# Kernel tuning notes

Measured on AMD Instinct MI355X. Metric: run time of the kernel, lower is better.

## Reference

```python
import jax, jax.numpy as jnp
import numpy as np

LN2 = float(np.log(2.0))

def ssp(x):
    # ShiftedSoftplus: softplus(x) - log(2)
    return jax.nn.softplus(x) - LN2

N_NODES = 40000
N_EDGES = 640000
HIDDEN = 128
N_FILTERS = 128
N_GAUSS = 50
CUTOFF = 10.0

def setup_inputs() -> dict:
    key = jax.random.key(0)
    ks = jax.random.split(key, 12)
    s = 0.05
    x = jax.random.normal(ks[0], (N_NODES, HIDDEN), dtype=jnp.float32)
    edge_index = jax.random.randint(ks[1], (2, N_EDGES), 0, N_NODES)
    edge_weight = jax.random.uniform(ks[2], (N_EDGES,), dtype=jnp.float32) * CUTOFF
    edge_attr = jax.random.normal(ks[3], (N_EDGES, N_GAUSS), dtype=jnp.float32)
    # filter MLP params (Linear(num_gaussians,num_filters), ssp, Linear(num_filters,num_filters))
    mlp_w1 = jax.random.normal(ks[4], (N_FILTERS, N_GAUSS), dtype=jnp.float32) * s
    mlp_b1 = jnp.zeros((N_FILTERS,), dtype=jnp.float32)
    mlp_w2 = jax.random.normal(ks[5], (N_FILTERS, N_FILTERS), dtype=jnp.float32) * s
    mlp_b2 = jnp.zeros((N_FILTERS,), dtype=jnp.float32)
    # CFConv linears: lin1 (no bias), lin2 (bias)
    lin1_w = jax.random.normal(ks[6], (N_FILTERS, HIDDEN), dtype=jnp.float32) * s
    lin2_w = jax.random.normal(ks[7], (HIDDEN, N_FILTERS), dtype=jnp.float32) * s
    lin2_b = jnp.zeros((HIDDEN,), dtype=jnp.float32)
    # output linear
    lin_w = jax.random.normal(ks[8], (HIDDEN, HIDDEN), dtype=jnp.float32) * s
    lin_b = jnp.zeros((HIDDEN,), dtype=jnp.float32)
    return {
        "x": x, "edge_index": edge_index, "edge_weight": edge_weight, "edge_attr": edge_attr,
        "mlp_w1": mlp_w1, "mlp_b1": mlp_b1, "mlp_w2": mlp_w2, "mlp_b2": mlp_b2,
        "lin1_w": lin1_w, "lin2_w": lin2_w, "lin2_b": lin2_b,
        "lin_w": lin_w, "lin_b": lin_b,
    }

def reference(x, edge_index, edge_weight, edge_attr,
              mlp_w1, mlp_b1, mlp_w2, mlp_b2,
              lin1_w, lin2_w, lin2_b, lin_w, lin_b):
    src, dst = edge_index[0], edge_index[1]
    # cosine envelope
    C = 0.5 * (jnp.cos(edge_weight * jnp.pi / CUTOFF) + 1.0)  # (E,)
    # filter MLP on Gaussian-smeared distances
    W = ssp(edge_attr @ mlp_w1.T + mlp_b1) @ mlp_w2.T + mlp_b2  # (E, F)
    W = W * C[:, None]
    # CFConv: lin1 -> gather x_j -> multiply -> scatter-add -> lin2
    h = x @ lin1_w.T                                            # (N, F)
    msg = h[src] * W                                            # (E, F)
    agg = jax.ops.segment_sum(msg, dst, num_segments=x.shape[0])  # (N, F)
    h2 = agg @ lin2_w.T + lin2_b                                # (N, H)
    # activation + output projection
    out = ssp(h2) @ lin_w.T + lin_b                             # (N, H)
    return out
```

## Files before the change

### kernel.cpp

```cpp
#include <hip/hip_runtime.h>
#include <math.h>

#define LN2F 0.69314718055994531f

typedef _Float16 v8hf __attribute__((ext_vector_type(8)));
typedef _Float16 v2hf __attribute__((ext_vector_type(2)));
typedef float    v4f  __attribute__((ext_vector_type(4)));

__device__ __forceinline__ float ssp_fast(float x) {
    float e = __expf(-fabsf(x));
    return fmaxf(x, 0.f) + __logf(1.f + e) - LN2F;
}

__global__ __launch_bounds__(256)
void prep_kernel(const float* __restrict__ w1, const float* __restrict__ w2,
                 const float* __restrict__ l1w, const float* __restrict__ l2w,
                 const float* __restrict__ lw,
                 _Float16* __restrict__ w1f, _Float16* __restrict__ w2f,
                 _Float16* __restrict__ l1f, _Float16* __restrict__ l2f,
                 _Float16* __restrict__ lwf)
{
    int idx = blockIdx.x * 256 + threadIdx.x;
    if (idx < 8192) {
        int i = idx & 7, lane = (idx >> 3) & 63, ks = (idx >> 9) & 1, nt = idx >> 10;
        int r = nt * 16 + (lane & 15);
        int k = ks * 32 + (lane >> 4) * 8 + i;
        w1f[idx] = (k < 50) ? (_Float16)w1[r * 50 + k] : (_Float16)0.f;
        return;
    }
    int o = idx - 8192;
    if (o >= 4 * 16384) return;
    int which = o >> 14;
    int p = o & 16383;
    int i = p & 7, lane = (p >> 3) & 63, ks = (p >> 9) & 3, nt = p >> 11;
    int r = nt * 16 + (lane & 15);
    int k = ks * 32 + (lane >> 4) * 8 + i;
    const float* src = (which == 0) ? w2 : (which == 1) ? l1w : (which == 2) ? l2w : lw;
    _Float16* dst   = (which == 0) ? w2f : (which == 1) ? l1f : (which == 2) ? l2f : lwf;
    dst[p] = (_Float16)src[r * 128 + k];
}

__global__ __launch_bounds__(256)
void h_gemm_kernel(const float* __restrict__ X, const _Float16* __restrict__ Wf,
                   float* __restrict__ Y, int M)
{
    const int tid = threadIdx.x, lane = tid & 63, wv = tid >> 6;
    const int l15 = lane & 15, quad = lane >> 4;
    const int mb = blockIdx.x * 64 + wv * 16;

    const int mA = (mb + l15 < M) ? (mb + l15) : (M - 1);
    v8hf a[4];
    #pragma unroll
    for (int ks = 0; ks < 4; ++ks) {
        const float4* xp = (const float4*)&X[(size_t)mA * 128 + ks * 32 + quad * 8];
        float4 x0 = xp[0], x1 = xp[1];
        v8hf t = {(_Float16)x0.x, (_Float16)x0.y, (_Float16)x0.z, (_Float16)x0.w,
                  (_Float16)x1.x, (_Float16)x1.y, (_Float16)x1.z, (_Float16)x1.w};
        a[ks] = t;
    }
    #pragma unroll
    for (int nt = 0; nt < 8; ++nt) {
        v4f acc = {0.f, 0.f, 0.f, 0.f};
        #pragma unroll
        for (int ks = 0; ks < 4; ++ks) {
            const v8hf b = *(const v8hf*)&Wf[((nt * 4 + ks) * 64 + lane) * 8];
            acc = __builtin_amdgcn_mfma_f32_16x16x32_f16(a[ks], b, acc, 0, 0, 0);
        }
        const int col = nt * 16 + l15;
        #pragma unroll
        for (int r = 0; r < 4; ++r) {
            int row = mb + quad * 4 + r;
            if (row < M) Y[(size_t)row * 128 + col] = acc[r];
        }
    }
}

__global__ __launch_bounds__(256)
void fused_out_kernel(const float* __restrict__ agg, const _Float16* __restrict__ l2f,
                      const float* __restrict__ l2b, const _Float16* __restrict__ lwf,
                      const float* __restrict__ lb, float* __restrict__ out, int M)
{
    __shared__ __align__(16) _Float16 Sh[64 * 138];
    const int tid = threadIdx.x, lane = tid & 63, wv = tid >> 6;
    const int l15 = lane & 15, quad = lane >> 4;
    const int m0 = wv * 16;
    const int gbase = blockIdx.x * 64;

    const int mA = (gbase + m0 + l15 < M) ? (gbase + m0 + l15) : (M - 1);
    v8hf a[4];
    #pragma unroll
    for (int ks = 0; ks < 4; ++ks) {
        const float4* xp = (const float4*)&agg[(size_t)mA * 128 + ks * 32 + quad * 8];
        float4 x0 = xp[0], x1 = xp[1];
        v8hf t = {(_Float16)x0.x, (_Float16)x0.y, (_Float16)x0.z, (_Float16)x0.w,
                  (_Float16)x1.x, (_Float16)x1.y, (_Float16)x1.z, (_Float16)x1.w};
        a[ks] = t;
    }
    #pragma unroll
    for (int nt = 0; nt < 8; ++nt) {
        v4f acc = {0.f, 0.f, 0.f, 0.f};
        #pragma unroll
        for (int ks = 0; ks < 4; ++ks) {
            const v8hf b = *(const v8hf*)&l2f[((nt * 4 + ks) * 64 + lane) * 8];
            acc = __builtin_amdgcn_mfma_f32_16x16x32_f16(a[ks], b, acc, 0, 0, 0);
        }
        const float bj = l2b[nt * 16 + l15];
        #pragma unroll
        for (int r = 0; r < 4; ++r)
            Sh[(m0 + quad * 4 + r) * 138 + nt * 16 + l15] =
                (_Float16)ssp_fast(acc[r] + bj);
    }
    v8hf ua[4];
    #pragma unroll
    for (int ks = 0; ks < 4; ++ks)
        ua[ks] = *(const v8hf*)&Sh[(m0 + l15) * 138 + ks * 32 + quad * 8];

    #pragma unroll
    for (int nt = 0; nt < 8; ++nt) {
        v4f acc = {0.f, 0.f, 0.f, 0.f};
        #pragma unroll
        for (int ks = 0; ks < 4; ++ks) {
            const v8hf b = *(const v8hf*)&lwf[((nt * 4 + ks) * 64 + lane) * 8];
            acc = __builtin_amdgcn_mfma_f32_16x16x32_f16(ua[ks], b, acc, 0, 0, 0);
        }
        const int col = nt * 16 + l15;
        const float bj = lb[col];
        #pragma unroll
        for (int r = 0; r < 4; ++r) {
            int row = gbase + m0 + quad * 4 + r;
            if (row < M) out[(size_t)row * 128 + col] = acc[r] + bj;
        }
    }
}

template<int MODE>
__global__ __launch_bounds__(256, 5)
void edge_kernel(const float* __restrict__ attr,
                 const float* __restrict__ ew,
                 const int* __restrict__ srcI,
                 const int* __restrict__ dstI,
                 const _Float16* __restrict__ w1f,
                 const _Float16* __restrict__ w2f,
                 const float* __restrict__ b1,
                 const float* __restrict__ b2,
                 const float* __restrict__ h,
                 float* __restrict__ agg,
                 float* __restrict__ msg32,
                 _Float16* __restrict__ msg16,
                 int E)
{
    __shared__ __align__(16) _Float16 Af[64 * 64];
    __shared__ __align__(16) _Float16 Uh[64 * 138];

    const int tid = threadIdx.x;
    const int e_base = blockIdx.x * 64;
    const int lane = tid & 63, wv = tid >> 6;
    const int m0 = wv * 16, l15 = lane & 15, quad = lane >> 4;

    float cC[4]; const float* hrow[4]; float* arow[4]; bool val[4]; int eidx[4];
    #pragma unroll
    for (int r = 0; r < 4; ++r) {
        int eg = e_base + m0 + quad * 4 + r;
        val[r] = eg < E;
        eidx[r] = eg;
        int e = val[r] ? eg : (E - 1);
        cC[r] = 0.5f * (__cosf(ew[e] * 0.31415926535897932f) + 1.f);
        hrow[r] = h + (size_t)srcI[e] * 128;
        if constexpr (MODE == 0) arow[r] = agg + (size_t)dstI[e] * 128;
    }

    for (int idx = tid; idx < 4096; idx += 256) {
        int r = idx >> 6, g = idx & 63;
        int e = e_base + r;
        float v = (g < 50 && e < E) ? attr[(size_t)e * 50 + g] : 0.f;
        Af[((((r >> 4) * 2 + (g >> 5)) * 64) + (((g & 31) >> 3) * 16) + (r & 15)) * 8
           + (g & 7)] = (_Float16)v;
    }
    __syncthreads();

    float hv[8][4];
    #pragma unroll
    for (int nt = 0; nt < 8; ++nt)
        #pragma unroll
        for (int r = 0; r < 4; ++r)
            hv[nt][r] = hrow[r][nt * 16 + l15];

    const v8hf a0 = *(const v8hf*)&Af[((wv * 2 + 0) * 64 + lane) * 8];
    const v8hf a1 = *(const v8hf*)&Af[((wv * 2 + 1) * 64 + lane) * 8];
    #pragma unroll
    for (int nt = 0; nt < 8; ++nt) {
        v4f acc = {0.f, 0.f, 0.f, 0.f};
        const v8hf bA = *(const v8hf*)&w1f[((nt * 2 + 0) * 64 + lane) * 8];
        const v8hf bB = *(const v8hf*)&w1f[((nt * 2 + 1) * 64 + lane) * 8];
        acc = __builtin_amdgcn_mfma_f32_16x16x32_f16(a0, bA, acc, 0, 0, 0);
        acc = __builtin_amdgcn_mfma_f32_16x16x32_f16(a1, bB, acc, 0, 0, 0);
        const float bj = b1[nt * 16 + l15];
        #pragma unroll
        for (int r = 0; r < 4; ++r)
            Uh[(m0 + quad * 4 + r) * 138 + nt * 16 + l15] =
                (_Float16)ssp_fast(acc[r] + bj);
    }

    v8hf ua[4];
    #pragma unroll
    for (int ks = 0; ks < 4; ++ks)
        ua[ks] = *(const v8hf*)&Uh[(m0 + l15) * 138 + ks * 32 + quad * 8];

    #pragma unroll
    for (int nt = 0; nt < 8; ++nt) {
        v4f acc = {0.f, 0.f, 0.f, 0.f};
        #pragma unroll
        for (int ks = 0; ks < 4; ++ks) {
            const v8hf b = *(const v8hf*)&w2f[((nt * 4 + ks) * 64 + lane) * 8];
            acc = __builtin_amdgcn_mfma_f32_16x16x32_f16(ua[ks], b, acc, 0, 0, 0);
        }
        const int col = nt * 16 + l15;
        const float bj = b2[col];
        #pragma unroll
        for (int r = 0; r < 4; ++r) {
            if (val[r]) {
                float m = (acc[r] + bj) * cC[r] * hv[nt][r];
                if constexpr (MODE == 0)
                    atomicAdd(&arow[r][col], m);
                else if constexpr (MODE == 1)
                    msg32[(size_t)eidx[r] * 128 + col] = m;
                else
                    msg16[(size_t)eidx[r] * 128 + col] = (_Float16)m;
            }
        }
    }
}

__global__ __launch_bounds__(256)
void hist_kernel(const int* __restrict__ dst, int* __restrict__ counts, int E)
{
    int i = blockIdx.x * 256 + threadIdx.x;
    const int stride = gridDim.x * 256;
    for (; i < E; i += stride) atomicAdd(&counts[dst[i]], 1);
}

__global__ __launch_bounds__(256)
void scan1_kernel(int* __restrict__ data, int* __restrict__ bsum, int N)
{
    __shared__ int wsum[4];
    const int t = threadIdx.x, lane = t & 63, wv = t >> 6;
    const int base = blockIdx.x * 1024 + t * 4;
    int v0 = 0, v1 = 0, v2 = 0, v3 = 0;
    if (base + 0 < N) v0 = data[base + 0];
    if (base + 1 < N) v1 = data[base + 1];
    if (base + 2 < N) v2 = data[base + 2];
    if (base + 3 < N) v3 = data[base + 3];
    const int s = v0 + v1 + v2 + v3;
    int sc = s;
    #pragma unroll
    for (int d = 1; d < 64; d <<= 1) {
        int o = __shfl_up(sc, d);
        if (lane >= d) sc += o;
    }
    if (lane == 63) wsum[wv] = sc;
    __syncthreads();
    int wo = 0;
    for (int j = 0; j < wv; ++j) wo += wsum[j];
    int run = wo + (sc - s);
    if (base + 0 < N) data[base + 0] = run; run += v0;
    if (base + 1 < N) data[base + 1] = run; run += v1;
    if (base + 2 < N) data[base + 2] = run; run += v2;
    if (base + 3 < N) data[base + 3] = run; run += v3;
    if (t == 255) bsum[blockIdx.x] = wo + sc;
}

__global__ __launch_bounds__(256)
void scan2_kernel(int* __restrict__ offs, const int* __restrict__ bsum,
                  int* __restrict__ cur, int N, int E)
{
    int add = 0;
    for (int j = 0; j < (int)blockIdx.x; ++j) add += bsum[j];
    const int base = blockIdx.x * 1024 + threadIdx.x * 4;
    #pragma unroll
    for (int r = 0; r < 4; ++r) {
        int i = base + r;
        if (i < N) { int o = offs[i] + add; offs[i] = o; cur[i] = o; }
    }
    if (blockIdx.x == 0 && threadIdx.x == 0) offs[N] = E;
}

__global__ __launch_bounds__(256)
void scatter_kernel(const int* __restrict__ dst, int* __restrict__ cur,
                    int* __restrict__ perm, int E)
{
    int i = blockIdx.x * 256 + threadIdx.x;
    const int stride = gridDim.x * 256;
    for (; i < E; i += stride) {
        int p = atomicAdd(&cur[dst[i]], 1);
        perm[p] = i;
    }
}

template<int MODE>
__global__ __launch_bounds__(256)
void gather_kernel(const float* __restrict__ msg32, const _Float16* __restrict__ msg16,
                   const int* __restrict__ offs, const int* __restrict__ perm,
                   float* __restrict__ agg, int N)
{
    const int lane = threadIdx.x & 63, wv = threadIdx.x >> 6;
    const int n = blockIdx.x * 4 + wv;
    if (n >= N) return;
    const int s = offs[n], e = offs[n + 1];
    float ax0 = 0.f, ay0 = 0.f, ax1 = 0.f, ay1 = 0.f;
    for (int k0 = s; k0 < e; k0 += 64) {
        const int pv = (k0 + lane < e) ? perm[k0 + lane] : 0;
        const int cnt = min(64, e - k0);
        int k = 0;
        for (; k + 1 < cnt; k += 2) {
            const int e0 = __shfl(pv, k);
            const int e1 = __shfl(pv, k + 1);
            if constexpr (MODE == 1) {
                const float2 m0 = *(const float2*)&msg32[(size_t)e0 * 128 + lane * 2];
                const float2 m1 = *(const float2*)&msg32[(size_t)e1 * 128 + lane * 2];
                ax0 += m0.x; ay0 += m0.y; ax1 += m1.x; ay1 += m1.y;
            } else {
                const v2hf m0 = *(const v2hf*)&msg16[(size_t)e0 * 128 + lane * 2];
                const v2hf m1 = *(const v2hf*)&msg16[(size_t)e1 * 128 + lane * 2];
                ax0 += (float)m0[0]; ay0 += (float)m0[1];
                ax1 += (float)m1[0]; ay1 += (float)m1[1];
            }
        }
        if (k < cnt) {
            const int e0 = __shfl(pv, k);
            if constexpr (MODE == 1) {
                const float2 m0 = *(const float2*)&msg32[(size_t)e0 * 128 + lane * 2];
                ax0 += m0.x; ay0 += m0.y;
            } else {
                const v2hf m0 = *(const v2hf*)&msg16[(size_t)e0 * 128 + lane * 2];
                ax0 += (float)m0[0]; ay0 += (float)m0[1];
            }
        }
    }
    float2 o; o.x = ax0 + ax1; o.y = ay0 + ay1;
    *(float2*)&agg[(size_t)n * 128 + lane * 2] = o;
}

extern "C" void kernel_launch(void* const* d_in, const int* in_sizes, int n_in,
                              void* d_out, int out_size, void* d_ws, size_t ws_size,
                              hipStream_t stream)
{
    const float* x   = (const float*)d_in[0];
    const int*   ei  = (const int*)  d_in[1];
    const float* ew  = (const float*)d_in[2];
    const float* ea  = (const float*)d_in[3];
    const float* w1  = (const float*)d_in[4];
    const float* b1  = (const float*)d_in[5];
    const float* w2  = (const float*)d_in[6];
    const float* b2  = (const float*)d_in[7];
    const float* l1w = (const float*)d_in[8];
    const float* l2w = (const float*)d_in[9];
    const float* l2b = (const float*)d_in[10];
    const float* lw  = (const float*)d_in[11];
    const float* lb  = (const float*)d_in[12];

    const int N = in_sizes[0] / 128;
    const int E = in_sizes[2];
    const int NB = (N + 1023) / 1024;

    char* base = (char*)d_ws;
    size_t off = 0;
    auto take = [&](size_t bytes) -> char* {
        char* r = base + off;
        off = (off + bytes + 255) & ~(size_t)255;
        return r;
    };
    float*    hbuf = (float*)   take((size_t)N * 128 * 4);
    float*    agg  = (float*)   take((size_t)N * 128 * 4);
    _Float16* w1f  = (_Float16*)take(8192 * 2);
    _Float16* w2f  = (_Float16*)take(16384 * 2);
    _Float16* l1f  = (_Float16*)take(16384 * 2);
    _Float16* l2f  = (_Float16*)take(16384 * 2);
    _Float16* lwf  = (_Float16*)take(16384 * 2);
    int*      offs = (int*)     take((size_t)(N + 1) * 4);
    int*      cur  = (int*)     take((size_t)N * 4);
    int*      bsum = (int*)     take((size_t)NB * 4);
    int*      perm = (int*)     take((size_t)E * 4);
    const size_t base_bytes = off;

    int mode;
    if      (ws_size >= base_bytes + (size_t)E * 128 * 4) mode = 1;
    else if (ws_size >= base_bytes + (size_t)E * 128 * 2) mode = 2;
    else                                                  mode = 0;
    float*    msg32 = (float*)   (base + off);
    _Float16* msg16 = (_Float16*)(base + off);

    const int nb = (N + 63) / 64;
    const int eb = (E + 63) / 64;
    const int tb = (E + 255) / 256;

    prep_kernel<<<288, 256, 0, stream>>>(w1, w2, l1w, l2w, lw,
                                         w1f, w2f, l1f, l2f, lwf);
    h_gemm_kernel<<<nb, 256, 0, stream>>>(x, l1f, hbuf, N);

    if (mode == 0) {
        hipMemsetAsync(agg, 0, (size_t)N * 128 * sizeof(float), stream);
        edge_kernel<0><<<eb, 256, 0, stream>>>(ea, ew, ei, ei + E, w1f, w2f, b1, b2,
                                               hbuf, agg, nullptr, nullptr, E);
    } else {
        hipMemsetAsync(offs, 0, (size_t)(N + 1) * sizeof(int), stream);
        hist_kernel<<<tb, 256, 0, stream>>>(ei + E, offs, E);
        scan1_kernel<<<NB, 256, 0, stream>>>(offs, bsum, N);
        scan2_kernel<<<NB, 256, 0, stream>>>(offs, bsum, cur, N, E);
        scatter_kernel<<<tb, 256, 0, stream>>>(ei + E, cur, perm, E);
        if (mode == 1) {
            edge_kernel<1><<<eb, 256, 0, stream>>>(ea, ew, ei, ei + E, w1f, w2f, b1, b2,
                                                   hbuf, nullptr, msg32, nullptr, E);
            gather_kernel<1><<<(N + 3) / 4, 256, 0, stream>>>(msg32, nullptr, offs, perm,
                                                              agg, N);
        } else {
            edge_kernel<2><<<eb, 256, 0, stream>>>(ea, ew, ei, ei + E, w1f, w2f, b1, b2,
                                                   hbuf, nullptr, nullptr, msg16, E);
            gather_kernel<2><<<(N + 3) / 4, 256, 0, stream>>>(nullptr, msg16, offs, perm,
                                                              agg, N);
        }
    }
    fused_out_kernel<<<nb, 256, 0, stream>>>(agg, l2f, l2b, lwf, lb, (float*)d_out, N);
}
```

Measured before the change: 606.7 us.

## Write edge messages in dst-sorted order so gather reads contiguously

The edge kernel now processes edges in destination-sorted permuted order, reading attr/ew/src through perm, and writes messages at their sorted position. The gather kernel then streams contiguous message rows per node instead of indirect perm lookups, with 4-way unrolled accumulation. The h_gemm and fused_out kernels are split over a second grid dimension over output column tiles to raise parallelism, at the cost of fused_out recomputing the first GEMM twice. The edge kernel now does scattered reads of edge_attr rows and the fp16 message fallback path is removed.

```diff
diff --git a/kernel.cpp b/kernel.cpp
--- a/kernel.cpp
+++ b/kernel.cpp
@@ -4,7 +4,6 @@
 #define LN2F 0.69314718055994531f
 
 typedef _Float16 v8hf __attribute__((ext_vector_type(8)));
-typedef _Float16 v2hf __attribute__((ext_vector_type(2)));
 typedef float    v4f  __attribute__((ext_vector_type(4)));
 
 __device__ __forceinline__ float ssp_fast(float x) {
@@ -47,6 +46,7 @@
     const int tid = threadIdx.x, lane = tid & 63, wv = tid >> 6;
     const int l15 = lane & 15, quad = lane >> 4;
     const int mb = blockIdx.x * 64 + wv * 16;
+    const int nt0 = blockIdx.y * 4;
 
     const int mA = (mb + l15 < M) ? (mb + l15) : (M - 1);
     v8hf a[4];
@@ -59,7 +59,7 @@
         a[ks] = t;
     }
     #pragma unroll
-    for (int nt = 0; nt < 8; ++nt) {
+    for (int nt = nt0; nt < nt0 + 4; ++nt) {
         v4f acc = {0.f, 0.f, 0.f, 0.f};
         #pragma unroll
         for (int ks = 0; ks < 4; ++ks) {
@@ -85,6 +85,7 @@
     const int l15 = lane & 15, quad = lane >> 4;
     const int m0 = wv * 16;
     const int gbase = blockIdx.x * 64;
+    const int nt0 = blockIdx.y * 4;
 
     const int mA = (gbase + m0 + l15 < M) ? (gbase + m0 + l15) : (M - 1);
     v8hf a[4];
@@ -116,7 +117,7 @@
         ua[ks] = *(const v8hf*)&Sh[(m0 + l15) * 138 + ks * 32 + quad * 8];
 
     #pragma unroll
-    for (int nt = 0; nt < 8; ++nt) {
+    for (int nt = nt0; nt < nt0 + 4; ++nt) {
         v4f acc = {0.f, 0.f, 0.f, 0.f};
         #pragma unroll
         for (int ks = 0; ks < 4; ++ks) {
@@ -133,21 +134,18 @@
     }
 }
 
-template<int MODE>
-__global__ __launch_bounds__(256, 5)
-void edge_kernel(const float* __restrict__ attr,
-                 const float* __restrict__ ew,
-                 const int* __restrict__ srcI,
-                 const int* __restrict__ dstI,
-                 const _Float16* __restrict__ w1f,
-                 const _Float16* __restrict__ w2f,
-                 const float* __restrict__ b1,
-                 const float* __restrict__ b2,
-                 const float* __restrict__ h,
-                 float* __restrict__ agg,
-                 float* __restrict__ msg32,
-                 _Float16* __restrict__ msg16,
-                 int E)
+__global__ __launch_bounds__(256, 6)
+void edge_perm_kernel(const float* __restrict__ attr,
+                      const float* __restrict__ ew,
+                      const int* __restrict__ srcI,
+                      const int* __restrict__ perm,
+                      const _Float16* __restrict__ w1f,
+                      const _Float16* __restrict__ w2f,
+                      const float* __restrict__ b1,
+                      const float* __restrict__ b2,
+                      const float* __restrict__ h,
+                      float* __restrict__ msg,
+                      int E)
 {
     __shared__ __align__(16) _Float16 Af[64 * 64];
     __shared__ __align__(16) _Float16 Uh[64 * 138];
@@ -157,18 +155,98 @@
     const int lane = tid & 63, wv = tid >> 6;
     const int m0 = wv * 16, l15 = lane & 15, quad = lane >> 4;
 
-    float cC[4]; const float* hrow[4]; float* arow[4]; bool val[4]; int eidx[4];
+    float cC[4]; const float* hrow[4]; bool val[4];
+    #pragma unroll
+    for (int r = 0; r < 4; ++r) {
+        int p = e_base + m0 + quad * 4 + r;
+        val[r] = p < E;
+        int pe = perm[val[r] ? p : (E - 1)];
+        cC[r] = 0.5f * (__cosf(ew[pe] * 0.31415926535897932f) + 1.f);
+        hrow[r] = h + (size_t)srcI[pe] * 128;
+    }
+
+    for (int idx = tid; idx < 4096; idx += 256) {
+        int r = idx >> 6, g = idx & 63;
+        int e = e_base + r;
+        int pe = perm[(e < E) ? e : (E - 1)];
+        float v = (g < 50 && e < E) ? attr[(size_t)pe * 50 + g] : 0.f;
+        Af[((((r >> 4) * 2 + (g >> 5)) * 64) + (((g & 31) >> 3) * 16) + (r & 15)) * 8
+           + (g & 7)] = (_Float16)v;
+    }
+    __syncthreads();
+
+    float hv[8][4];
+    #pragma unroll
+    for (int nt = 0; nt < 8; ++nt)
+        #pragma unroll
+        for (int r = 0; r < 4; ++r)
+            hv[nt][r] = hrow[r][nt * 16 + l15];
+
+    const v8hf a0 = *(const v8hf*)&Af[((wv * 2 + 0) * 64 + lane) * 8];
+    const v8hf a1 = *(const v8hf*)&Af[((wv * 2 + 1) * 64 + lane) * 8];
+    #pragma unroll
+    for (int nt = 0; nt < 8; ++nt) {
+        v4f acc = {0.f, 0.f, 0.f, 0.f};
+        const v8hf bA = *(const v8hf*)&w1f[((nt * 2 + 0) * 64 + lane) * 8];
+        const v8hf bB = *(const v8hf*)&w1f[((nt * 2 + 1) * 64 + lane) * 8];
+        acc = __builtin_amdgcn_mfma_f32_16x16x32_f16(a0, bA, acc, 0, 0, 0);
+        acc = __builtin_amdgcn_mfma_f32_16x16x32_f16(a1, bB, acc, 0, 0, 0);
+        const float bj = b1[nt * 16 + l15];
+        #pragma unroll
+        for (int r = 0; r < 4; ++r)
+            Uh[(m0 + quad * 4 + r) * 138 + nt * 16 + l15] =
+                (_Float16)ssp_fast(acc[r] + bj);
+    }
+
+    v8hf ua[4];
+    #pragma unroll
+    for (int ks = 0; ks < 4; ++ks)
+        ua[ks] = *(const v8hf*)&Uh[(m0 + l15) * 138 + ks * 32 + quad * 8];
+
+    #pragma unroll
+    for (int nt = 0; nt < 8; ++nt) {
+        v4f acc = {0.f, 0.f, 0.f, 0.f};
+        #pragma unroll
+        for (int ks = 0; ks < 4; ++ks) {
+            const v8hf b = *(const v8hf*)&w2f[((nt * 4 + ks) * 64 + lane) * 8];
+            acc = __builtin_amdgcn_mfma_f32_16x16x32_f16(ua[ks], b, acc, 0, 0, 0);
+        }
+        const int col = nt * 16 + l15;
+        const float bj = b2[col];
+        #pragma unroll
+        for (int r = 0; r < 4; ++r) {
+            if (val[r]) {
+                int p = e_base + m0 + quad * 4 + r;
+                msg[(size_t)p * 128 + col] = (acc[r] + bj) * cC[r] * hv[nt][r];
+            }
+        }
+    }
+}
+
+__global__ __launch_bounds__(256, 5)
+void edge_legacy_kernel(const float* __restrict__ attr, const float* __restrict__ ew,
+                        const int* __restrict__ srcI, const int* __restrict__ dstI,
+                        const _Float16* __restrict__ w1f, const _Float16* __restrict__ w2f,
+                        const float* __restrict__ b1, const float* __restrict__ b2,
+                        const float* __restrict__ h, float* __restrict__ agg, int E)
+{
+    __shared__ __align__(16) _Float16 Af[64 * 64];
+    __shared__ __align__(16) _Float16 Uh[64 * 138];
+    const int tid = threadIdx.x;
+    const int e_base = blockIdx.x * 64;
+    const int lane = tid & 63, wv = tid >> 6;
+    const int m0 = wv * 16, l15 = lane & 15, quad = lane >> 4;
+
+    float cC[4]; const float* hrow[4]; float* arow[4]; bool val[4];
     #pragma unroll
     for (int r = 0; r < 4; ++r) {
         int eg = e_base + m0 + quad * 4 + r;
         val[r] = eg < E;
-        eidx[r] = eg;
         int e = val[r] ? eg : (E - 1);
         cC[r] = 0.5f * (__cosf(ew[e] * 0.31415926535897932f) + 1.f);
         hrow[r] = h + (size_t)srcI[e] * 128;
-        if constexpr (MODE == 0) arow[r] = agg + (size_t)dstI[e] * 128;
-    }
-
+        arow[r] = agg + (size_t)dstI[e] * 128;
+    }
     for (int idx = tid; idx < 4096; idx += 256) {
         int r = idx >> 6, g = idx & 63;
         int e = e_base + r;
@@ -177,7 +255,6 @@
            + (g & 7)] = (_Float16)v;
     }
     __syncthreads();
-
     float hv[8][4];
     #pragma unroll
     for (int nt = 0; nt < 8; ++nt)
@@ -200,12 +277,10 @@
             Uh[(m0 + quad * 4 + r) * 138 + nt * 16 + l15] =
                 (_Float16)ssp_fast(acc[r] + bj);
     }
-
     v8hf ua[4];
     #pragma unroll
     for (int ks = 0; ks < 4; ++ks)
         ua[ks] = *(const v8hf*)&Uh[(m0 + l15) * 138 + ks * 32 + quad * 8];
-
     #pragma unroll
     for (int nt = 0; nt < 8; ++nt) {
         v4f acc = {0.f, 0.f, 0.f, 0.f};
@@ -217,17 +292,8 @@
         const int col = nt * 16 + l15;
         const float bj = b2[col];
         #pragma unroll
-        for (int r = 0; r < 4; ++r) {
-            if (val[r]) {
-                float m = (acc[r] + bj) * cC[r] * hv[nt][r];
-                if constexpr (MODE == 0)
-                    atomicAdd(&arow[r][col], m);
-                else if constexpr (MODE == 1)
-                    msg32[(size_t)eidx[r] * 128 + col] = m;
-                else
-                    msg16[(size_t)eidx[r] * 128 + col] = (_Float16)m;
-            }
-        }
+        for (int r = 0; r < 4; ++r)
+            if (val[r]) atomicAdd(&arow[r][col], (acc[r] + bj) * cC[r] * hv[nt][r]);
     }
 }
 
@@ -296,47 +362,34 @@
     }
 }
 
-template<int MODE>
-__global__ __launch_bounds__(256)
-void gather_kernel(const float* __restrict__ msg32, const _Float16* __restrict__ msg16,
-                   const int* __restrict__ offs, const int* __restrict__ perm,
+__global__ __launch_bounds__(256)
+void gather_kernel(const float* __restrict__ msg, const int* __restrict__ offs,
                    float* __restrict__ agg, int N)
 {
     const int lane = threadIdx.x & 63, wv = threadIdx.x >> 6;
     const int n = blockIdx.x * 4 + wv;
     if (n >= N) return;
     const int s = offs[n], e = offs[n + 1];
+    const float* p = msg + (size_t)s * 128 + lane * 2;
     float ax0 = 0.f, ay0 = 0.f, ax1 = 0.f, ay1 = 0.f;
-    for (int k0 = s; k0 < e; k0 += 64) {
-        const int pv = (k0 + lane < e) ? perm[k0 + lane] : 0;
-        const int cnt = min(64, e - k0);
-        int k = 0;
-        for (; k + 1 < cnt; k += 2) {
-            const int e0 = __shfl(pv, k);
-            const int e1 = __shfl(pv, k + 1);
-            if constexpr (MODE == 1) {
-                const float2 m0 = *(const float2*)&msg32[(size_t)e0 * 128 + lane * 2];
-                const float2 m1 = *(const float2*)&msg32[(size_t)e1 * 128 + lane * 2];
-                ax0 += m0.x; ay0 += m0.y; ax1 += m1.x; ay1 += m1.y;
-            } else {
-                const v2hf m0 = *(const v2hf*)&msg16[(size_t)e0 * 128 + lane * 2];
-                const v2hf m1 = *(const v2hf*)&msg16[(size_t)e1 * 128 + lane * 2];
-                ax0 += (float)m0[0]; ay0 += (float)m0[1];
-                ax1 += (float)m1[0]; ay1 += (float)m1[1];
-            }
-        }
-        if (k < cnt) {
-            const int e0 = __shfl(pv, k);
-            if constexpr (MODE == 1) {
-                const float2 m0 = *(const float2*)&msg32[(size_t)e0 * 128 + lane * 2];
-                ax0 += m0.x; ay0 += m0.y;
-            } else {
-                const v2hf m0 = *(const v2hf*)&msg16[(size_t)e0 * 128 + lane * 2];
-                ax0 += (float)m0[0]; ay0 += (float)m0[1];
-            }
-        }
-    }
-    float2 o; o.x = ax0 + ax1; o.y = ay0 + ay1;
+    float ax2 = 0.f, ay2 = 0.f, ax3 = 0.f, ay3 = 0.f;
+    int k = s;
+    for (; k + 3 < e; k += 4) {
+        float2 m0 = *(const float2*)(p);
+        float2 m1 = *(const float2*)(p + 128);
+        float2 m2 = *(const float2*)(p + 256);
+        float2 m3 = *(const float2*)(p + 384);
+        p += 512;
+        ax0 += m0.x; ay0 += m0.y; ax1 += m1.x; ay1 += m1.y;
+        ax2 += m2.x; ay2 += m2.y; ax3 += m3.x; ay3 += m3.y;
+    }
+    for (; k < e; ++k) {
+        float2 m = *(const float2*)p; p += 128;
+        ax0 += m.x; ay0 += m.y;
+    }
+    float2 o;
+    o.x = (ax0 + ax1) + (ax2 + ax3);
+    o.y = (ay0 + ay1) + (ay2 + ay3);
     *(float2*)&agg[(size_t)n * 128 + lane * 2] = o;
 }
 
@@ -382,12 +435,8 @@
     int*      perm = (int*)     take((size_t)E * 4);
     const size_t base_bytes = off;
 
-    int mode;
-    if      (ws_size >= base_bytes + (size_t)E * 128 * 4) mode = 1;
-    else if (ws_size >= base_bytes + (size_t)E * 128 * 2) mode = 2;
-    else                                                  mode = 0;
-    float*    msg32 = (float*)   (base + off);
-    _Float16* msg16 = (_Float16*)(base + off);
+    const bool fits = ws_size >= base_bytes + (size_t)E * 128 * 4;
+    float* msg = (float*)(base + off);
 
     const int nb = (N + 63) / 64;
     const int eb = (E + 63) / 64;
@@ -395,29 +444,22 @@
 
     prep_kernel<<<288, 256, 0, stream>>>(w1, w2, l1w, l2w, lw,
                                          w1f, w2f, l1f, l2f, lwf);
-    h_gemm_kernel<<<nb, 256, 0, stream>>>(x, l1f, hbuf, N);
-
-    if (mode == 0) {
+    h_gemm_kernel<<<dim3(nb, 2), 256, 0, stream>>>(x, l1f, hbuf, N);
+
+    if (!fits) {
         hipMemsetAsync(agg, 0, (size_t)N * 128 * sizeof(float), stream);
-        edge_kernel<0><<<eb, 256, 0, stream>>>(ea, ew, ei, ei + E, w1f, w2f, b1, b2,
-                                               hbuf, agg, nullptr, nullptr, E);
+        edge_legacy_kernel<<<eb, 256, 0, stream>>>(ea, ew, ei, ei + E, w1f, w2f,
+                                                   b1, b2, hbuf, agg, E);
     } else {
         hipMemsetAsync(offs, 0, (size_t)(N + 1) * sizeof(int), stream);
         hist_kernel<<<tb, 256, 0, stream>>>(ei + E, offs, E);
         scan1_kernel<<<NB, 256, 0, stream>>>(offs, bsum, N);
         scan2_kernel<<<NB, 256, 0, stream>>>(offs, bsum, cur, N, E);
         scatter_kernel<<<tb, 256, 0, stream>>>(ei + E, cur, perm, E);
-        if (mode == 1) {
-            edge_kernel<1><<<eb, 256, 0, stream>>>(ea, ew, ei, ei + E, w1f, w2f, b1, b2,
-                                                   hbuf, nullptr, msg32, nullptr, E);
-            gather_kernel<1><<<(N + 3) / 4, 256, 0, stream>>>(msg32, nullptr, offs, perm,
-                                                              agg, N);
-        } else {
-            edge_kernel<2><<<eb, 256, 0, stream>>>(ea, ew, ei, ei + E, w1f, w2f, b1, b2,
-                                                   hbuf, nullptr, nullptr, msg16, E);
-            gather_kernel<2><<<(N + 3) / 4, 256, 0, stream>>>(nullptr, msg16, offs, perm,
-                                                              agg, N);
-        }
-    }
-    fused_out_kernel<<<nb, 256, 0, stream>>>(agg, l2f, l2b, lwf, lb, (float*)d_out, N);
-}
+        edge_perm_kernel<<<eb, 256, 0, stream>>>(ea, ew, ei, perm, w1f, w2f,
+                                                 b1, b2, hbuf, msg, E);
+        gather_kernel<<<(N + 3) / 4, 256, 0, stream>>>(msg, offs, agg, N);
+    }
+    fused_out_kernel<<<dim3(nb, 2), 256, 0, stream>>>(agg, l2f, l2b, lwf, lb,
+                                                      (float*)d_out, N);
+}
```

New measurement: 680.1 us. +12.1%, slower.
